# Performance work log

Measured on AMD Instinct MI355X. Metric: run time of the kernel, lower is better.

## Reference

```python
import jax, jax.numpy as jnp
import numpy as np

B, L, D, H = 2, 2048, 512, 8
SAMPLING_FACTOR = 5


def setup_inputs() -> dict:
    key = jax.random.key(0)
    ks = jax.random.split(key, 12)
    L_K = min(8000, L)
    log_L_K = int(np.ceil(np.log1p(L_K)))
    U_part = min(SAMPLING_FACTOR * L * log_L_K, L_K)  # = 2048
    inp = {
        'q': jax.random.normal(ks[0], (B, L, D), jnp.float32),
        'k': jax.random.normal(ks[1], (B, L, D), jnp.float32),
        'v': jax.random.normal(ks[2], (B, L, D), jnp.float32),
        'Wq': jax.random.normal(ks[3], (D, D), jnp.float32) * 0.02,
        'bq': jnp.zeros((D,), jnp.float32),
        'Wk': jax.random.normal(ks[4], (D, D), jnp.float32) * 0.02,
        'bk': jnp.zeros((D,), jnp.float32),
        'Wv': jax.random.normal(ks[5], (D, D), jnp.float32) * 0.02,
        'bv': jnp.zeros((D,), jnp.float32),
        'Wo': jax.random.normal(ks[6], (D, D), jnp.float32) * 0.02,
        'bo': jnp.zeros((D,), jnp.float32),
        'index_sample': jax.random.randint(ks[7], (U_part,), 0, L_K, jnp.int32),
    }
    return inp


def _prob_sparse(qh, Kh, Vh, index_sample):
    # qh, Kh, Vh: [B, H, L, d]
    L_K = min(8000, Kh.shape[2])  # K_sample = K[:, :8000]; L_K = its length
    L_Q = qh.shape[2]
    Ks = Kh[:, :, index_sample, :]                                  # [B,H,U,d]
    QKs = jnp.einsum('bhqd,bhkd->bhqk', qh, Ks)                     # [B,H,Lq,U]
    # M = max - sum/L_K  (source divides by L_K, not U_part)
    M = QKs.max(axis=-1) - QKs.sum(axis=-1) / L_K                   # [B,H,Lq]
    u = min(SAMPLING_FACTOR * int(np.ceil(np.log1p(L_Q))), L_Q)     # = 40
    _, M_top = jax.lax.top_k(-M, u)                                 # topk(largest=False)
    Q_red = jnp.take_along_axis(qh, M_top[..., None], axis=2)       # [B,H,u,d]
    d_k = qh.shape[-1]
    scores = jnp.einsum('bhqd,bhkd->bhqk', Q_red, Kh) / jnp.sqrt(jnp.asarray(d_k, qh.dtype))
    probs = jax.nn.softmax(scores, axis=-1)
    out = jnp.einsum('bhqk,bhkd->bhqd', probs, Vh)                  # [B,H,u,d]
    return out, scores


def reference(q, k, v, Wq, bq, Wk, bk, Wv, bv, Wo, bo, index_sample):
    qp = q @ Wq.T + bq
    kp = k @ Wk.T + bk
    vp = v @ Wv.T + bv
    Bsz, Lq, Dm = qp.shape
    d = Dm // H
    # faithful to source: q is view'd to [B,H,Lq,d] WITHOUT transpose
    qh = qp.reshape(Bsz, H, Lq, d)
    kh = kp.reshape(Bsz, -1, H, d).transpose(0, 2, 1, 3)
    vh = vp.reshape(Bsz, -1, H, d).transpose(0, 2, 1, 3)
    out, _ = _prob_sparse(qh, kh, vh, index_sample)
    u = out.shape[2]
    out = out.transpose(0, 2, 1, 3).reshape(Bsz, u, Dm)             # concat
    return out @ Wo.T + bo                                          # [B,u,D]
```

## Files before the change

### kernel.cpp

```cpp
#include <hip/hip_runtime.h>
#include <math.h>

#define B_ 2
#define L_ 2048
#define D_ 512
#define H_ 8
#define DH 64
#define NS 2048
#define NU 40
#define BHD (L_*D_)
#define QHS (L_*DH)
#define WSPM 786432

typedef __attribute__((ext_vector_type(8))) short bf16x8;
typedef __attribute__((ext_vector_type(4))) float f32x4;

__device__ inline float4 ld4(const float* p) { return *reinterpret_cast<const float4*>(p); }

__device__ inline unsigned short hi16(float x) { return (unsigned short)(__float_as_uint(x) >> 16); }
__device__ inline float trunchf(float x) { return __uint_as_float(__float_as_uint(x) & 0xFFFF0000u); }
__device__ inline void tsplit(float x, unsigned short& hs, unsigned short& ms, unsigned short& ls) {
  float h = trunchf(x); hs = hi16(x);
  float r = x - h;
  float m = trunchf(r); ms = hi16(r);
  float r2 = r - m;
  ls = hi16(r2);
}

__global__ __launch_bounds__(256) void wsplit(const float* __restrict__ Wq,
                                              const float* __restrict__ Wk,
                                              const float* __restrict__ Wv,
                                              unsigned short* __restrict__ dst,
                                              int matArg) {
  const int mat = (matArg >= 0) ? matArg : (int)blockIdx.y;
  const float* W = (mat == 0) ? Wq : (mat == 1) ? Wk : Wv;
  unsigned short* d = dst + ((matArg >= 0) ? 0 : (size_t)mat * WSPM);
  const int t = threadIdx.x;
  const int nt = blockIdx.x >> 3, g16 = blockIdx.x & 7;
  const int kc = t >> 4, lr = t & 15;
  const int n = nt*128 + g16*16 + lr;
  const float* src = W + (size_t)n*512 + kc*32;
  float xs[32];
#pragma unroll
  for (int i = 0; i < 8; ++i) {
    float4 v4 = ld4(src + 4*i);
    xs[4*i] = v4.x; xs[4*i+1] = v4.y; xs[4*i+2] = v4.z; xs[4*i+3] = v4.w;
  }
  unsigned short Hs[32], Ms[32], Ls[32];
#pragma unroll
  for (int e = 0; e < 32; ++e) tsplit(xs[e], Hs[e], Ms[e], Ls[e]);
#pragma unroll
  for (int p = 0; p < 3; ++p) {
    const unsigned short* sp = (p == 0) ? Hs : (p == 1) ? Ms : Ls;
    unsigned short* base = d + ((size_t)((p*4 + nt)*8 + g16)*16 + kc)*512;
#pragma unroll
    for (int lg = 0; lg < 4; ++lg) {
      union { bf16x8 v; unsigned short u[8]; } P;
#pragma unroll
      for (int e = 0; e < 8; ++e) P.u[e] = sp[lg*8 + e];
      *reinterpret_cast<bf16x8*>(base + (lr + 16*lg)*8) = P.v;
    }
  }
}

__global__ __launch_bounds__(256, 2) void proj_pipe(
    const float* __restrict__ qa, const float* __restrict__ ka, const float* __restrict__ va,
    const unsigned short* __restrict__ wsp,
    const float* __restrict__ bq, const float* __restrict__ bk, const float* __restrict__ bv,
    float* __restrict__ qp, float* __restrict__ kp, float* __restrict__ vp,
    int matArg)
{
  __shared__ __align__(16) unsigned short a3[2][3][128][36];
  const int t = threadIdx.x;
  const int mat = (matArg >= 0) ? matArg : (int)blockIdx.z;
  const float* A    = (mat == 0) ? qa : (mat == 1) ? ka : va;
  const float* bias = (mat == 0) ? bq : (mat == 1) ? bk : bv;
  float* C          = (mat == 0) ? qp : (mat == 1) ? kp : vp;
  const unsigned short* wspm = wsp + ((matArg >= 0) ? 0 : (size_t)mat * WSPM);
  const int m0 = blockIdx.x * 128, nt = blockIdx.y;
  const int w = t >> 6, l = t & 63;
  const int wm = w >> 1, wn = w & 1;
  const int lr = l & 15, lg = l >> 4;
  const int srow = t >> 1, sc0 = (t & 1) * 16;
  const float* aRow = A + (size_t)(m0 + srow) * 512 + sc0;

  f32x4 acc[4][4];
#pragma unroll
  for (int i = 0; i < 4; ++i)
#pragma unroll
    for (int j = 0; j < 4; ++j) acc[i][j] = (f32x4){0.f, 0.f, 0.f, 0.f};

#define LOADW(dst, kcv)                                                        \
  _Pragma("unroll")                                                            \
  for (int p = 0; p < 3; ++p)                                                  \
    _Pragma("unroll")                                                          \
    for (int ni = 0; ni < 4; ++ni)                                             \
      dst[p][ni] = *reinterpret_cast<const bf16x8*>(                           \
          wspm + ((size_t)((p*4 + nt)*8 + wn*4 + ni)*16 + (kcv))*512 + l*8);

#define SPLITSTORE(r0, r1, r2, r3, buf)                                        \
  {                                                                            \
    float xs[16] = {r0.x, r0.y, r0.z, r0.w, r1.x, r1.y, r1.z, r1.w,            \
                    r2.x, r2.y, r2.z, r2.w, r3.x, r3.y, r3.z, r3.w};           \
    _Pragma("unroll")                                                          \
    for (int hh = 0; hh < 2; ++hh) {                                           \
      union { bf16x8 v; unsigned short u[8]; } H, M, L;                        \
      _Pragma("unroll")                                                        \
      for (int e = 0; e < 8; ++e) tsplit(xs[hh*8 + e], H.u[e], M.u[e], L.u[e]);\
      *reinterpret_cast<bf16x8*>(&a3[buf][0][srow][sc0 + 8*hh]) = H.v;         \
      *reinterpret_cast<bf16x8*>(&a3[buf][1][srow][sc0 + 8*hh]) = M.v;         \
      *reinterpret_cast<bf16x8*>(&a3[buf][2][srow][sc0 + 8*hh]) = L.v;         \
    }                                                                          \
  }

#define MFMA6(buf, bw)                                                         \
  __builtin_amdgcn_s_setprio(1);                                               \
  _Pragma("unroll")                                                            \
  for (int mi = 0; mi < 4; ++mi) {                                             \
    bf16x8 a0 = *reinterpret_cast<const bf16x8*>(&a3[buf][0][wm*64 + mi*16 + lr][lg*8]); \
    bf16x8 a1 = *reinterpret_cast<const bf16x8*>(&a3[buf][1][wm*64 + mi*16 + lr][lg*8]); \
    bf16x8 a2 = *reinterpret_cast<const bf16x8*>(&a3[buf][2][wm*64 + mi*16 + lr][lg*8]); \
    _Pragma("unroll")                                                          \
    for (int ni = 0; ni < 4; ++ni) {                                           \
      acc[mi][ni] = __builtin_amdgcn_mfma_f32_16x16x32_bf16(a0, bw[0][ni], acc[mi][ni], 0, 0, 0); \
      acc[mi][ni] = __builtin_amdgcn_mfma_f32_16x16x32_bf16(a0, bw[1][ni], acc[mi][ni], 0, 0, 0); \
      acc[mi][ni] = __builtin_amdgcn_mfma_f32_16x16x32_bf16(a1, bw[0][ni], acc[mi][ni], 0, 0, 0); \
      acc[mi][ni] = __builtin_amdgcn_mfma_f32_16x16x32_bf16(a1, bw[1][ni], acc[mi][ni], 0, 0, 0); \
      acc[mi][ni] = __builtin_amdgcn_mfma_f32_16x16x32_bf16(a0, bw[2][ni], acc[mi][ni], 0, 0, 0); \
      acc[mi][ni] = __builtin_amdgcn_mfma_f32_16x16x32_bf16(a2, bw[0][ni], acc[mi][ni], 0, 0, 0); \
    }                                                                          \
  }                                                                            \
  __builtin_amdgcn_s_setprio(0);

  float4 arA0 = ld4(aRow), arA1 = ld4(aRow + 4), arA2 = ld4(aRow + 8), arA3 = ld4(aRow + 12);
  bf16x8 bwA[3][4], bwB[3][4];
  LOADW(bwA, 0);
  float4 arB0, arB1, arB2, arB3;

  for (int kc = 0; kc < 16; kc += 2) {
    SPLITSTORE(arA0, arA1, arA2, arA3, 0);
    __syncthreads();
    if (kc < 15) {
      const float* src = aRow + (kc+1)*32;
      arB0 = ld4(src); arB1 = ld4(src + 4); arB2 = ld4(src + 8); arB3 = ld4(src + 12);
      LOADW(bwB, kc+1);
    }
    MFMA6(0, bwA);
    SPLITSTORE(arB0, arB1, arB2, arB3, 1);
    __syncthreads();
    if (kc + 2 < 16) {
      const float* src = aRow + (kc+2)*32;
      arA0 = ld4(src); arA1 = ld4(src + 4); arA2 = ld4(src + 8); arA3 = ld4(src + 12);
      LOADW(bwA, kc+2);
    }
    MFMA6(1, bwB);
  }
#undef LOADW
#undef SPLITSTORE
#undef MFMA6

#pragma unroll
  for (int mi = 0; mi < 4; ++mi)
#pragma unroll
    for (int ni = 0; ni < 4; ++ni) {
      const int gn = nt*128 + wn*64 + ni*16 + lr;
      const float bv_ = bias[gn];
#pragma unroll
      for (int r = 0; r < 4; ++r) {
        const int gm = m0 + wm*64 + mi*16 + lg*4 + r;
        C[(size_t)gm * 512 + gn] = acc[mi][ni][r] + bv_;
      }
    }
}

__global__ __launch_bounds__(1024) void ksum_kernel(const float* __restrict__ kp,
                                                    const int* __restrict__ idx,
                                                    float* __restrict__ ksum) {
  __shared__ float part[16][64];
  const int bh = blockIdx.x;
  const int b = bh >> 3, h = bh & 7;
  const int t = threadIdx.x;
  const int sg = t >> 6, j = t & 63;
  const float* kbase = kp + (size_t)b*BHD + h*DH;
  float a = 0.f;
  for (int s = sg*128; s < sg*128 + 128; ++s)
    a += kbase[(size_t)idx[s]*512 + j];
  part[sg][j] = a;
  __syncthreads();
  if (t < 64) {
    float s = 0.f;
#pragma unroll
    for (int i = 0; i < 16; ++i) s += part[i][t];
    ksum[bh*64 + t] = s;
  }
}

__global__ __launch_bounds__(256) void dedupe(const int* __restrict__ idx,
                                              int* __restrict__ ulist,
                                              int* __restrict__ ucnt) {
  __shared__ unsigned bm[64];
  __shared__ int base[64];
  __shared__ int total;
  const int t = threadIdx.x;
  if (t < 64) bm[t] = 0;
  __syncthreads();
#pragma unroll
  for (int c = 0; c < 8; ++c) {
    const int v = idx[c*256 + t];
    atomicOr(&bm[v >> 5], 1u << (v & 31));
  }
  __syncthreads();
  if (t < 64) {
    const int cnt = __popc(bm[t]);
    int inc = cnt;
#pragma unroll
    for (int off = 1; off < 64; off <<= 1) {
      const int nb = __shfl_up(inc, off);
      if (t >= off) inc += nb;
    }
    base[t] = inc - cnt;
    if (t == 63) total = inc;
  }
  __syncthreads();
  if (t < 64) {
    unsigned w = bm[t];
    int pos = base[t];
    while (w) {
      const int b = __ffs(w) - 1;
      w &= w - 1;
      ulist[pos++] = t*32 + b;
    }
  }
  __syncthreads();
  const int U = total;
  const int nt = (U + 127) >> 7;
  const int padded = nt << 7;
  const int first = ulist[0];
  for (int p = U + t; p < padded; p += 256) ulist[p] = first;
  if (t == 0) ucnt[0] = nt;
}

__global__ __launch_bounds__(256, 2) void m_kernel(const float* __restrict__ qp,
                                                   const float* __restrict__ kp,
                                                   const int* __restrict__ ulist,
                                                   const int* __restrict__ ucnt,
                                                   float* __restrict__ Mp) {
  __shared__ __align__(16) unsigned short k3[3][128][72];
  const int t = threadIdx.x;
  const int bid = blockIdx.x;
  const int bh = bid >> 6, qt = (bid >> 3) & 7, ks = bid & 7;
  const int b = bh >> 3, h = bh & 7;
  const int w = t >> 6, l = t & 63;
  const int lr = l & 15;
  const int lg = l >> 4;

  bf16x8 qf[4][2][3];
  {
    const float* qbase = qp + (size_t)b*BHD + (size_t)h*QHS + (size_t)(qt*256 + w*64 + lr) * 64 + lg*8;
#pragma unroll
    for (int mi = 0; mi < 4; ++mi)
#pragma unroll
      for (int c = 0; c < 2; ++c) {
        const float* src = qbase + mi*16*64 + c*32;
        float4 x0 = ld4(src), x1 = ld4(src + 4);
        float xs[8] = {x0.x, x0.y, x0.z, x0.w, x1.x, x1.y, x1.z, x1.w};
        union { bf16x8 v; unsigned short u[8]; } H, M, L;
#pragma unroll
        for (int e = 0; e < 8; ++e) tsplit(xs[e], H.u[e], M.u[e], L.u[e]);
        qf[mi][c][0] = H.v; qf[mi][c][1] = M.v; qf[mi][c][2] = L.v;
      }
  }

  const float* kbase = kp + (size_t)b*BHD + h*DH;
  const int ntiles = ucnt[0];
  const int srow = t >> 1, sh = (t & 1) * 32;

  float4 vst[8];
  if (ks < ntiles) {
    const int kr = ulist[ks*128 + srow];
    const float* src = kbase + (size_t)kr * 512 + sh;
#pragma unroll
    for (int i = 0; i < 8; ++i) vst[i] = ld4(src + 4*i);
  }

  float mx[4][4];
#pragma unroll
  for (int mi = 0; mi < 4; ++mi)
#pragma unroll
    for (int r = 0; r < 4; ++r) mx[mi][r] = -INFINITY;

  for (int ti = ks; ti < ntiles; ti += 8) {
    __syncthreads();
    {
#pragma unroll
      for (int e2 = 0; e2 < 4; ++e2) {
        union { bf16x8 v; unsigned short u[8]; } H, M, L;
        float xs[8] = {vst[2*e2].x, vst[2*e2].y, vst[2*e2].z, vst[2*e2].w,
                       vst[2*e2+1].x, vst[2*e2+1].y, vst[2*e2+1].z, vst[2*e2+1].w};
#pragma unroll
        for (int e = 0; e < 8; ++e) tsplit(xs[e], H.u[e], M.u[e], L.u[e]);
        *reinterpret_cast<bf16x8*>(&k3[0][srow][sh + 8*e2]) = H.v;
        *reinterpret_cast<bf16x8*>(&k3[1][srow][sh + 8*e2]) = M.v;
        *reinterpret_cast<bf16x8*>(&k3[2][srow][sh + 8*e2]) = L.v;
      }
    }
    if (ti + 8 < ntiles) {
      const int kr = ulist[(ti+8)*128 + srow];
      const float* src = kbase + (size_t)kr * 512 + sh;
#pragma unroll
      for (int i = 0; i < 8; ++i) vst[i] = ld4(src + 4*i);
    }
    __syncthreads();

    for (int n2 = 0; n2 < 4; ++n2) {
      bf16x8 bf[2][3][2];
#pragma unroll
      for (int ns = 0; ns < 2; ++ns)
#pragma unroll
        for (int p = 0; p < 3; ++p)
#pragma unroll
          for (int c = 0; c < 2; ++c)
            bf[ns][p][c] = *reinterpret_cast<const bf16x8*>(&k3[p][n2*32 + ns*16 + lr][c*32 + lg*8]);
      __builtin_amdgcn_s_setprio(1);
#pragma unroll
      for (int mi = 0; mi < 4; ++mi)
#pragma unroll
        for (int ns = 0; ns < 2; ++ns) {
          f32x4 acc = {0.f, 0.f, 0.f, 0.f};
#pragma unroll
          for (int c = 0; c < 2; ++c) acc = __builtin_amdgcn_mfma_f32_16x16x32_bf16(qf[mi][c][0], bf[ns][0][c], acc, 0, 0, 0);
#pragma unroll
          for (int c = 0; c < 2; ++c) acc = __builtin_amdgcn_mfma_f32_16x16x32_bf16(qf[mi][c][0], bf[ns][1][c], acc, 0, 0, 0);
#pragma unroll
          for (int c = 0; c < 2; ++c) acc = __builtin_amdgcn_mfma_f32_16x16x32_bf16(qf[mi][c][1], bf[ns][0][c], acc, 0, 0, 0);
#pragma unroll
          for (int c = 0; c < 2; ++c) acc = __builtin_amdgcn_mfma_f32_16x16x32_bf16(qf[mi][c][1], bf[ns][1][c], acc, 0, 0, 0);
#pragma unroll
          for (int c = 0; c < 2; ++c) acc = __builtin_amdgcn_mfma_f32_16x16x32_bf16(qf[mi][c][0], bf[ns][2][c], acc, 0, 0, 0);
#pragma unroll
          for (int c = 0; c < 2; ++c) acc = __builtin_amdgcn_mfma_f32_16x16x32_bf16(qf[mi][c][2], bf[ns][0][c], acc, 0, 0, 0);
#pragma unroll
          for (int r = 0; r < 4; ++r) mx[mi][r] = fmaxf(mx[mi][r], acc[r]);
        }
      __builtin_amdgcn_s_setprio(0);
    }
  }

#pragma unroll
  for (int mi = 0; mi < 4; ++mi)
#pragma unroll
    for (int r = 0; r < 4; ++r) {
      float v = mx[mi][r];
      v = fmaxf(v, __shfl_xor(v, 1));
      v = fmaxf(v, __shfl_xor(v, 2));
      v = fmaxf(v, __shfl_xor(v, 4));
      v = fmaxf(v, __shfl_xor(v, 8));
      if (lr == 0)
        Mp[ks*32768 + bh*2048 + qt*256 + w*64 + mi*16 + lg*4 + r] = v;
    }
}

__global__ __launch_bounds__(256) void topk_kernel(const float* __restrict__ qp,
                                                   const float* __restrict__ ksum,
                                                   const float* __restrict__ Mp,
                                                   int* __restrict__ Mtop) {
  __shared__ float ks_s[64];
  __shared__ unsigned hist[256];
  __shared__ int wsum[4];
  __shared__ unsigned bitmap[64];
  __shared__ unsigned long long comb[NU];
  __shared__ int s_sel, s_rem, s_cnt;
  const int bh = blockIdx.x;
  const int b = bh >> 3, h = bh & 7;
  const int t = threadIdx.x;
  if (t < 64) ks_s[t] = ksum[bh*64 + t];
  __syncthreads();

  unsigned mykey[8];
#pragma unroll
  for (int c = 0; c < 8; ++c) {
    const int qi = c * 256 + t;
    const float* qrow = qp + (size_t)b*BHD + (size_t)h*QHS + (size_t)qi * 64;
    float dot = 0.f;
#pragma unroll
    for (int cc = 0; cc < 16; ++cc) {
      float4 q4 = ld4(qrow + 4 * cc);
      dot += q4.x * ks_s[4*cc + 0];
      dot += q4.y * ks_s[4*cc + 1];
      dot += q4.z * ks_s[4*cc + 2];
      dot += q4.w * ks_s[4*cc + 3];
    }
    float mxv = Mp[bh*2048 + qi];
#pragma unroll
    for (int s = 1; s < 8; ++s) mxv = fmaxf(mxv, Mp[s*32768 + bh*2048 + qi]);
    const float m = mxv - dot * (1.0f/2048.0f);
    const unsigned u = __float_as_uint(m);
    mykey[c] = (u >> 31) ? ~u : (u | 0x80000000u);
  }

  unsigned prefMask = 0u, prefVal = 0u;
  int rem = NU;
  for (int shift = 24; shift >= 0; shift -= 8) {
    hist[t] = 0;
    __syncthreads();
#pragma unroll
    for (int c = 0; c < 8; ++c) {
      const unsigned key = mykey[c];
      if ((key & prefMask) == prefVal)
        atomicAdd(&hist[(key >> shift) & 255], 1u);
    }
    __syncthreads();
    const int binc = (int)hist[t];
    int inc = binc;
#pragma unroll
    for (int off = 1; off < 64; off <<= 1) {
      const int nb = __shfl_up(inc, off);
      if ((t & 63) >= off) inc += nb;
    }
    if ((t & 63) == 63) wsum[t >> 6] = inc;
    __syncthreads();
    int wadd = 0;
    for (int w2 = 0; w2 < (t >> 6); ++w2) wadd += wsum[w2];
    const int incl = inc + wadd;
    const int excl = incl - binc;
    if (excl < rem && rem <= incl) { s_sel = t; s_rem = rem - excl; }
    __syncthreads();
    prefVal |= ((unsigned)s_sel) << shift;
    prefMask |= 0xFFu << shift;
    rem = s_rem;
    __syncthreads();
  }
  const unsigned T = prefVal;

  if (t < 64) bitmap[t] = 0;
  if (t == 0) s_cnt = 0;
  __syncthreads();
#pragma unroll
  for (int c = 0; c < 8; ++c) {
    const unsigned key = mykey[c];
    const int qi = c * 256 + t;
    if (key < T) {
      const int pos = atomicAdd(&s_cnt, 1);
      comb[pos] = ((unsigned long long)key << 11) | (unsigned)qi;
    } else if (key == T) {
      atomicOr(&bitmap[qi >> 5], 1u << (qi & 31));
    }
  }
  __syncthreads();
  if (t == 0) {
    int need = rem, cpos = s_cnt;
    for (int wd = 0; wd < 64 && need > 0; ++wd) {
      unsigned bits = bitmap[wd];
      while (bits && need > 0) {
        const int bit = __ffs(bits) - 1;
        bits &= bits - 1;
        comb[cpos++] = ((unsigned long long)T << 11) | (unsigned)(wd*32 + bit);
        --need;
      }
    }
  }
  __syncthreads();

  if (t < 64) {
    const unsigned long long mine = (t < NU) ? comb[t] : ~0ULL;
    int rank = 0;
#pragma unroll
    for (int step = 1; step < 64; ++step) {
      const unsigned long long other = __shfl(mine, (t + step) & 63);
      rank += (other < mine) ? 1 : 0;
    }
    if (t < NU) Mtop[bh*NU + rank] = (int)(mine & 0x7FFu);
  }
}

__global__ __launch_bounds__(256) void flash_partial(const float* __restrict__ qp,
                                                     const float* __restrict__ kp,
                                                     const float* __restrict__ vp,
                                                     const int* __restrict__ Mtop,
                                                     float* __restrict__ pm,
                                                     float* __restrict__ pl,
                                                     float* __restrict__ pacc) {
  __shared__ float qr[NU][65];
  __shared__ float kv[64][65];
  __shared__ float sl[NU][65];
  __shared__ float ms[NU], ls[NU], fs[NU];
  const int bid = blockIdx.x;
  const int bh = bid >> 4, kt = bid & 15;
  const int b = bh >> 3, h = bh & 7;
  const int t = threadIdx.x;
  const int g = t >> 6, j = t & 63;
  const int r4 = t >> 2, sub = t & 3;

  {
    const float* qbase = qp + (size_t)b*BHD + (size_t)h*QHS;
#pragma unroll
    for (int r = 0; r < 10; ++r) {
      const int q = g*10 + r;
      qr[q][j] = qbase[(size_t)Mtop[bh*NU + q]*64 + j];
    }
  }
  if (t < NU) { ms[t] = -INFINITY; ls[t] = 0.f; }
  float acc[10];
#pragma unroll
  for (int r = 0; r < 10; ++r) acc[r] = 0.f;

  const float* kbase = kp + (size_t)b*BHD + h*DH;
  const float* vbase = vp + (size_t)b*BHD + h*DH;
  const int srow = t >> 2, scb = (t & 3)*16;

  for (int st = 0; st < 2; ++st) {
    const int kb = kt*128 + st*64;
    __syncthreads();
    {
      const float* src = kbase + (size_t)(kb + srow)*512 + scb;
#pragma unroll
      for (int i = 0; i < 4; ++i) {
        float4 v = ld4(src + 4*i);
        kv[srow][scb + 4*i + 0] = v.x;
        kv[srow][scb + 4*i + 1] = v.y;
        kv[srow][scb + 4*i + 2] = v.z;
        kv[srow][scb + 4*i + 3] = v.w;
      }
    }
    __syncthreads();
    {
      float sv[10];
#pragma unroll
      for (int r = 0; r < 10; ++r) {
        const int q = g*10 + r;
        float s = 0.f;
#pragma unroll 8
        for (int jj = 0; jj < 64; ++jj) s += qr[q][jj]*kv[j][jj];
        sv[r] = s * 0.125f;
      }
#pragma unroll
      for (int r = 0; r < 10; ++r) sl[g*10 + r][j] = sv[r];
    }
    __syncthreads();
    float4 vst[4];
    {
      const float* src = vbase + (size_t)(kb + srow)*512 + scb;
#pragma unroll
      for (int i = 0; i < 4; ++i) vst[i] = ld4(src + 4*i);
    }
    if (r4 < NU) {
      float tm = -INFINITY;
#pragma unroll
      for (int c = 0; c < 16; ++c) tm = fmaxf(tm, sl[r4][sub*16 + c]);
      tm = fmaxf(tm, __shfl_xor(tm, 1));
      tm = fmaxf(tm, __shfl_xor(tm, 2));
      const float nm = fmaxf(ms[r4], tm);
      if (sub == 0) { fs[r4] = expf(ms[r4] - nm); ms[r4] = nm; }
    }
    __syncthreads();
    {
#pragma unroll
      for (int r = 0; r < 10; ++r) {
        const int q = g*10 + r;
        acc[r] *= fs[q];
        sl[q][j] = expf(sl[q][j] - ms[q]);
      }
#pragma unroll
      for (int i = 0; i < 4; ++i) {
        kv[srow][scb + 4*i + 0] = vst[i].x;
        kv[srow][scb + 4*i + 1] = vst[i].y;
        kv[srow][scb + 4*i + 2] = vst[i].z;
        kv[srow][scb + 4*i + 3] = vst[i].w;
      }
    }
    __syncthreads();
    if (r4 < NU) {
      float s = 0.f;
#pragma unroll
      for (int c = 0; c < 16; ++c) s += sl[r4][sub*16 + c];
      s += __shfl_xor(s, 1);
      s += __shfl_xor(s, 2);
      if (sub == 0) ls[r4] = ls[r4]*fs[r4] + s;
    }
    {
#pragma unroll 4
      for (int kk = 0; kk < 64; ++kk) {
        const float vv = kv[kk][j];
#pragma unroll
        for (int r = 0; r < 10; ++r) acc[r] += sl[g*10 + r][kk]*vv;
      }
    }
  }
  __syncthreads();
  const size_t base = (size_t)(bh*16 + kt)*NU;
  if (t < NU) { pm[base + t] = ms[t]; pl[base + t] = ls[t]; }
#pragma unroll
  for (int r = 0; r < 10; ++r)
    pacc[(base + g*10 + r)*64 + j] = acc[r];
}

__global__ __launch_bounds__(256) void flash_combine(const float* __restrict__ pm,
                                                     const float* __restrict__ pl,
                                                     const float* __restrict__ pacc,
                                                     float* __restrict__ outc) {
  const int t = threadIdx.x;
  const int qg = t >> 6, j = t & 63;
  const int bh = blockIdx.x / 10;
  const int q  = (blockIdx.x % 10)*4 + qg;
  const int b = bh >> 3, h = bh & 7;
  float m = -INFINITY;
#pragma unroll
  for (int kt = 0; kt < 16; ++kt) m = fmaxf(m, pm[(size_t)(bh*16 + kt)*NU + q]);
  float Lsum = 0.f, num = 0.f;
#pragma unroll
  for (int kt = 0; kt < 16; ++kt) {
    const size_t base = (size_t)(bh*16 + kt)*NU;
    const float w = expf(pm[base + q] - m);
    Lsum += w * pl[base + q];
    num  += w * pacc[(base + q)*64 + j];
  }
  outc[(size_t)(b*NU + q)*512 + h*64 + j] = num / Lsum;
}

__global__ __launch_bounds__(256) void wo_gemm(const float* __restrict__ outc,
                                               const float* __restrict__ Wo,
                                               float* __restrict__ pwo) {
  __shared__ __align__(16) float a_t[80][68];
  __shared__ __align__(16) float w_t[64][68];
  const int t = threadIdx.x;
  const int ty = t >> 4, tx = t & 15;
  const int nt = blockIdx.x, ks = blockIdx.y;
  float acc[5][4];
#pragma unroll
  for (int i = 0; i < 5; ++i)
#pragma unroll
    for (int j = 0; j < 4; ++j) acc[i][j] = 0.f;

  for (int c = 0; c < 2; ++c) {
    const int kb = ks*128 + c*64;
    __syncthreads();
#pragma unroll
    for (int i = 0; i < 20; ++i) {
      const int fi = t + 256*i;
      const int row = fi >> 6, col = fi & 63;
      a_t[row][col] = outc[(size_t)row*512 + kb + col];
    }
#pragma unroll
    for (int i = 0; i < 16; ++i) {
      const int fi = t + 256*i;
      const int row = fi >> 6, col = fi & 63;
      w_t[row][col] = Wo[(size_t)(nt*64 + row)*512 + kb + col];
    }
    __syncthreads();
    for (int gq = 0; gq < 16; ++gq) {
      float4 av[5], wv[4];
#pragma unroll
      for (int i = 0; i < 5; ++i) av[i] = *reinterpret_cast<const float4*>(&a_t[ty + 16*i][4*gq]);
#pragma unroll
      for (int j = 0; j < 4; ++j) wv[j] = *reinterpret_cast<const float4*>(&w_t[tx + 16*j][4*gq]);
#pragma unroll
      for (int i = 0; i < 5; ++i)
#pragma unroll
        for (int j = 0; j < 4; ++j) {
          acc[i][j] += av[i].x * wv[j].x;
          acc[i][j] += av[i].y * wv[j].y;
          acc[i][j] += av[i].z * wv[j].z;
          acc[i][j] += av[i].w * wv[j].w;
        }
    }
  }
#pragma unroll
  for (int i = 0; i < 5; ++i)
#pragma unroll
    for (int j = 0; j < 4; ++j)
      pwo[ks*40960 + (size_t)(ty + 16*i)*512 + nt*64 + tx + 16*j] = acc[i][j];
}

__global__ __launch_bounds__(256) void wo_combine(const float* __restrict__ pwo,
                                                  const float* __restrict__ bo,
                                                  float* __restrict__ out) {
  const int gi = blockIdx.x*256 + threadIdx.x;
  const float4* p = reinterpret_cast<const float4*>(pwo);
  const float4 a = p[gi], b4 = p[10240 + gi], c4 = p[20480 + gi], d4 = p[30720 + gi];
  const float4 bb = ld4(bo + 4*(gi & 127));
  float4 o;
  o.x = a.x + b4.x + c4.x + d4.x + bb.x;
  o.y = a.y + b4.y + c4.y + d4.y + bb.y;
  o.z = a.z + b4.z + c4.z + d4.z + bb.z;
  o.w = a.w + b4.w + c4.w + d4.w + bb.w;
  reinterpret_cast<float4*>(out)[gi] = o;
}

extern "C" void kernel_launch(void* const* d_in, const int* in_sizes, int n_in,
                              void* d_out, int out_size, void* d_ws, size_t ws_size,
                              hipStream_t stream) {
  const float* q  = (const float*)d_in[0];
  const float* k  = (const float*)d_in[1];
  const float* v  = (const float*)d_in[2];
  const float* Wq = (const float*)d_in[3];
  const float* bq = (const float*)d_in[4];
  const float* Wk = (const float*)d_in[5];
  const float* bk = (const float*)d_in[6];
  const float* Wv = (const float*)d_in[7];
  const float* bv = (const float*)d_in[8];
  const float* Wo = (const float*)d_in[9];
  const float* bo = (const float*)d_in[10];
  const int*  idx = (const int*)d_in[11];

  float* ws   = (float*)d_ws;
  float* qp   = ws;
  float* kp   = ws + 2097152;
  float* vp   = ws + 4194304;
  float* ksum = ws + 6291456;
  int*   Mtop = (int*)(ws + 6292480);
  float* pm   = ws + 6293120;
  float* pl   = ws + 6303360;
  float* pacc = ws + 6313600;
  float* outc = ws + 6968960;
  float* Mp   = pm;
  float* pwo  = pm;
  unsigned short* wsp = (unsigned short*)(ws + 6291456);
  int* ulist = (int*)(ws + 6600000);
  int* ucnt  = ulist + 2048;

  const dim3 blk(256);
  const bool bigws = (ws_size >= (size_t)7471104 * 4);
  if (bigws) {
    wsplit<<<dim3(32, 3), blk, 0, stream>>>(Wq, Wk, Wv, wsp, -1);
    proj_pipe<<<dim3(32, 4, 3), blk, 0, stream>>>(q, k, v, wsp, bq, bk, bv, qp, kp, vp, -1);
  } else {
    for (int m = 0; m < 3; ++m) {
      wsplit<<<dim3(32, 1), blk, 0, stream>>>(Wq, Wk, Wv, wsp, m);
      proj_pipe<<<dim3(32, 4, 1), blk, 0, stream>>>(q, k, v, wsp, bq, bk, bv, qp, kp, vp, m);
    }
  }
  ksum_kernel<<<dim3(16), dim3(1024), 0, stream>>>(kp, idx, ksum);
  dedupe<<<dim3(1), blk, 0, stream>>>(idx, ulist, ucnt);
  m_kernel<<<dim3(1024), blk, 0, stream>>>(qp, kp, ulist, ucnt, Mp);
  topk_kernel<<<dim3(16), blk, 0, stream>>>(qp, ksum, Mp, Mtop);
  flash_partial<<<dim3(256), blk, 0, stream>>>(qp, kp, vp, Mtop, pm, pl, pacc);
  flash_combine<<<dim3(160), blk, 0, stream>>>(pm, pl, pacc, outc);
  wo_gemm<<<dim3(8, 4), blk, 0, stream>>>(outc, Wo, pwo);
  wo_combine<<<dim3(40), blk, 0, stream>>>(pwo, bo, (float*)d_out);
}
```

Before: 201.2 us.

## Widen projection tiles to 128x256 and drop index dedupe in max pass

Each projection block now computes a 128x256 output tile per wave pair (8 N-subtiles per wave), which halves the grid and raises A-tile reuse, at the cost of doubled accumulators and weight registers under launch_bounds(256,1). The dedupe kernel is removed. The M max pass now iterates over all 2048 sampled indices directly in 4 split-K slices of 512, instead of over the deduplicated unique list in 8 slices. This removes a serial single-block launch but does extra work on the duplicate indices (roughly 1300 unique out of 2048). The topk kernel now combines 4 partial maxima instead of 8.

```diff
diff --git a/kernel.cpp b/kernel.cpp
--- a/kernel.cpp
+++ b/kernel.cpp
@@ -63,7 +63,7 @@
   }
 }
 
-__global__ __launch_bounds__(256, 2) void proj_pipe(
+__global__ __launch_bounds__(256, 1) void proj_fat(
     const float* __restrict__ qa, const float* __restrict__ ka, const float* __restrict__ va,
     const unsigned short* __restrict__ wsp,
     const float* __restrict__ bq, const float* __restrict__ bk, const float* __restrict__ bv,
@@ -77,26 +77,27 @@
   const float* bias = (mat == 0) ? bq : (mat == 1) ? bk : bv;
   float* C          = (mat == 0) ? qp : (mat == 1) ? kp : vp;
   const unsigned short* wspm = wsp + ((matArg >= 0) ? 0 : (size_t)mat * WSPM);
-  const int m0 = blockIdx.x * 128, nt = blockIdx.y;
+  const int m0 = blockIdx.x * 128, ntb = blockIdx.y;
   const int w = t >> 6, l = t & 63;
   const int wm = w >> 1, wn = w & 1;
+  const int NT = ntb*2 + wn;
   const int lr = l & 15, lg = l >> 4;
   const int srow = t >> 1, sc0 = (t & 1) * 16;
   const float* aRow = A + (size_t)(m0 + srow) * 512 + sc0;
 
-  f32x4 acc[4][4];
+  f32x4 acc[4][8];
 #pragma unroll
   for (int i = 0; i < 4; ++i)
 #pragma unroll
-    for (int j = 0; j < 4; ++j) acc[i][j] = (f32x4){0.f, 0.f, 0.f, 0.f};
+    for (int j = 0; j < 8; ++j) acc[i][j] = (f32x4){0.f, 0.f, 0.f, 0.f};
 
 #define LOADW(dst, kcv)                                                        \
   _Pragma("unroll")                                                            \
   for (int p = 0; p < 3; ++p)                                                  \
     _Pragma("unroll")                                                          \
-    for (int ni = 0; ni < 4; ++ni)                                             \
+    for (int ni = 0; ni < 8; ++ni)                                             \
       dst[p][ni] = *reinterpret_cast<const bf16x8*>(                           \
-          wspm + ((size_t)((p*4 + nt)*8 + wn*4 + ni)*16 + (kcv))*512 + l*8);
+          wspm + ((size_t)((p*4 + NT)*8 + ni)*16 + (kcv))*512 + l*8);
 
 #define SPLITSTORE(r0, r1, r2, r3, buf)                                        \
   {                                                                            \
@@ -121,7 +122,7 @@
     bf16x8 a1 = *reinterpret_cast<const bf16x8*>(&a3[buf][1][wm*64 + mi*16 + lr][lg*8]); \
     bf16x8 a2 = *reinterpret_cast<const bf16x8*>(&a3[buf][2][wm*64 + mi*16 + lr][lg*8]); \
     _Pragma("unroll")                                                          \
-    for (int ni = 0; ni < 4; ++ni) {                                           \
+    for (int ni = 0; ni < 8; ++ni) {                                           \
       acc[mi][ni] = __builtin_amdgcn_mfma_f32_16x16x32_bf16(a0, bw[0][ni], acc[mi][ni], 0, 0, 0); \
       acc[mi][ni] = __builtin_amdgcn_mfma_f32_16x16x32_bf16(a0, bw[1][ni], acc[mi][ni], 0, 0, 0); \
       acc[mi][ni] = __builtin_amdgcn_mfma_f32_16x16x32_bf16(a1, bw[0][ni], acc[mi][ni], 0, 0, 0); \
@@ -133,7 +134,7 @@
   __builtin_amdgcn_s_setprio(0);
 
   float4 arA0 = ld4(aRow), arA1 = ld4(aRow + 4), arA2 = ld4(aRow + 8), arA3 = ld4(aRow + 12);
-  bf16x8 bwA[3][4], bwB[3][4];
+  bf16x8 bwA[3][8], bwB[3][8];
   LOADW(bwA, 0);
   float4 arB0, arB1, arB2, arB3;
 
@@ -162,8 +163,8 @@
 #pragma unroll
   for (int mi = 0; mi < 4; ++mi)
 #pragma unroll
-    for (int ni = 0; ni < 4; ++ni) {
-      const int gn = nt*128 + wn*64 + ni*16 + lr;
+    for (int ni = 0; ni < 8; ++ni) {
+      const int gn = NT*128 + ni*16 + lr;
       const float bv_ = bias[gn];
 #pragma unroll
       for (int r = 0; r < 4; ++r) {
@@ -195,60 +196,14 @@
   }
 }
 
-__global__ __launch_bounds__(256) void dedupe(const int* __restrict__ idx,
-                                              int* __restrict__ ulist,
-                                              int* __restrict__ ucnt) {
-  __shared__ unsigned bm[64];
-  __shared__ int base[64];
-  __shared__ int total;
-  const int t = threadIdx.x;
-  if (t < 64) bm[t] = 0;
-  __syncthreads();
-#pragma unroll
-  for (int c = 0; c < 8; ++c) {
-    const int v = idx[c*256 + t];
-    atomicOr(&bm[v >> 5], 1u << (v & 31));
-  }
-  __syncthreads();
-  if (t < 64) {
-    const int cnt = __popc(bm[t]);
-    int inc = cnt;
-#pragma unroll
-    for (int off = 1; off < 64; off <<= 1) {
-      const int nb = __shfl_up(inc, off);
-      if (t >= off) inc += nb;
-    }
-    base[t] = inc - cnt;
-    if (t == 63) total = inc;
-  }
-  __syncthreads();
-  if (t < 64) {
-    unsigned w = bm[t];
-    int pos = base[t];
-    while (w) {
-      const int b = __ffs(w) - 1;
-      w &= w - 1;
-      ulist[pos++] = t*32 + b;
-    }
-  }
-  __syncthreads();
-  const int U = total;
-  const int nt = (U + 127) >> 7;
-  const int padded = nt << 7;
-  const int first = ulist[0];
-  for (int p = U + t; p < padded; p += 256) ulist[p] = first;
-  if (t == 0) ucnt[0] = nt;
-}
-
 __global__ __launch_bounds__(256, 2) void m_kernel(const float* __restrict__ qp,
                                                    const float* __restrict__ kp,
-                                                   const int* __restrict__ ulist,
-                                                   const int* __restrict__ ucnt,
+                                                   const int* __restrict__ idx,
                                                    float* __restrict__ Mp) {
   __shared__ __align__(16) unsigned short k3[3][128][72];
   const int t = threadIdx.x;
   const int bid = blockIdx.x;
-  const int bh = bid >> 6, qt = (bid >> 3) & 7, ks = bid & 7;
+  const int bh = bid >> 5, qt = (bid >> 2) & 7, ks = bid & 3;
   const int b = bh >> 3, h = bh & 7;
   const int w = t >> 6, l = t & 63;
   const int lr = l & 15;
@@ -272,12 +227,12 @@
   }
 
   const float* kbase = kp + (size_t)b*BHD + h*DH;
-  const int ntiles = ucnt[0];
+  const int ib = ks * 512;
   const int srow = t >> 1, sh = (t & 1) * 32;
 
   float4 vst[8];
-  if (ks < ntiles) {
-    const int kr = ulist[ks*128 + srow];
+  {
+    const int kr = idx[ib + srow];
     const float* src = kbase + (size_t)kr * 512 + sh;
 #pragma unroll
     for (int i = 0; i < 8; ++i) vst[i] = ld4(src + 4*i);
@@ -289,7 +244,7 @@
 #pragma unroll
     for (int r = 0; r < 4; ++r) mx[mi][r] = -INFINITY;
 
-  for (int ti = ks; ti < ntiles; ti += 8) {
+  for (int tl = 0; tl < 4; ++tl) {
     __syncthreads();
     {
 #pragma unroll
@@ -304,8 +259,8 @@
         *reinterpret_cast<bf16x8*>(&k3[2][srow][sh + 8*e2]) = L.v;
       }
     }
-    if (ti + 8 < ntiles) {
-      const int kr = ulist[(ti+8)*128 + srow];
+    if (tl < 3) {
+      const int kr = idx[ib + (tl+1)*128 + srow];
       const float* src = kbase + (size_t)kr * 512 + sh;
 #pragma unroll
       for (int i = 0; i < 8; ++i) vst[i] = ld4(src + 4*i);
@@ -390,10 +345,9 @@
       dot += q4.z * ks_s[4*cc + 2];
       dot += q4.w * ks_s[4*cc + 3];
     }
-    float mxv = Mp[bh*2048 + qi];
-#pragma unroll
-    for (int s = 1; s < 8; ++s) mxv = fmaxf(mxv, Mp[s*32768 + bh*2048 + qi]);
-    const float m = mxv - dot * (1.0f/2048.0f);
+    const float mx2 = fmaxf(fmaxf(Mp[bh*2048 + qi], Mp[32768 + bh*2048 + qi]),
+                            fmaxf(Mp[65536 + bh*2048 + qi], Mp[98304 + bh*2048 + qi]));
+    const float m = mx2 - dot * (1.0f/2048.0f);
     const unsigned u = __float_as_uint(m);
     mykey[c] = (u >> 31) ? ~u : (u | 0x80000000u);
   }
@@ -715,23 +669,20 @@
   float* Mp   = pm;
   float* pwo  = pm;
   unsigned short* wsp = (unsigned short*)(ws + 6291456);
-  int* ulist = (int*)(ws + 6600000);
-  int* ucnt  = ulist + 2048;
 
   const dim3 blk(256);
   const bool bigws = (ws_size >= (size_t)7471104 * 4);
   if (bigws) {
     wsplit<<<dim3(32, 3), blk, 0, stream>>>(Wq, Wk, Wv, wsp, -1);
-    proj_pipe<<<dim3(32, 4, 3), blk, 0, stream>>>(q, k, v, wsp, bq, bk, bv, qp, kp, vp, -1);
+    proj_fat<<<dim3(32, 2, 3), blk, 0, stream>>>(q, k, v, wsp, bq, bk, bv, qp, kp, vp, -1);
   } else {
     for (int m = 0; m < 3; ++m) {
       wsplit<<<dim3(32, 1), blk, 0, stream>>>(Wq, Wk, Wv, wsp, m);
-      proj_pipe<<<dim3(32, 4, 1), blk, 0, stream>>>(q, k, v, wsp, bq, bk, bv, qp, kp, vp, m);
+      proj_fat<<<dim3(32, 2, 1), blk, 0, stream>>>(q, k, v, wsp, bq, bk, bv, qp, kp, vp, m);
     }
   }
   ksum_kernel<<<dim3(16), dim3(1024), 0, stream>>>(kp, idx, ksum);
-  dedupe<<<dim3(1), blk, 0, stream>>>(idx, ulist, ucnt);
-  m_kernel<<<dim3(1024), blk, 0, stream>>>(qp, kp, ulist, ucnt, Mp);
+  m_kernel<<<dim3(512), blk, 0, stream>>>(qp, kp, idx, Mp);
   topk_kernel<<<dim3(16), blk, 0, stream>>>(qp, ksum, Mp, Mtop);
   flash_partial<<<dim3(256), blk, 0, stream>>>(qp, kp, vp, Mtop, pm, pl, pacc);
   flash_combine<<<dim3(160), blk, 0, stream>>>(pm, pl, pacc, outc);
```

New measurement: 200.4 us. Within noise of the previous version (-0.4%).
